# Kernel tuning notes

Measured on AMD Instinct MI355X. Metric: run time of the kernel, lower is better.

Reference implementation:

```python
import jax, jax.numpy as jnp
import numpy as np

B, C, S, DIM = 8, 3, 1024, 768
H = 3
HD = DIM // H  # 256


def setup_inputs() -> dict:
    key = jax.random.key(0)
    ks = jax.random.split(key, 7)
    s = 1.0 / np.sqrt(HD)  # torch Linear default init scale
    return {
        "linear_embed": jax.random.normal(ks[0], (B, C, S, DIM), dtype=jnp.float32),
        "Wq": jax.random.uniform(ks[1], (H, HD, HD), jnp.float32, -s, s),
        "bq": jax.random.uniform(ks[2], (H, HD), jnp.float32, -s, s),
        "Wk": jax.random.uniform(ks[3], (H, HD, HD), jnp.float32, -s, s),
        "bk": jax.random.uniform(ks[4], (H, HD), jnp.float32, -s, s),
        "Wv": jax.random.uniform(ks[5], (H, HD, HD), jnp.float32, -s, s),
        "bv": jax.random.uniform(ks[6], (H, HD), jnp.float32, -s, s),
    }


def reference(linear_embed, Wq, bq, Wk, bk, Wv, bv):
    # Split last dim into heads: [B, C, S, H, HD]
    x = linear_embed.reshape(B, C, S, H, HD)
    # Per-head Linear: y = x @ W.T + b (torch convention, W is [out, in])
    q = jnp.einsum("bcshd,hed->bcshe", x, Wq) + bq
    k = jnp.einsum("bcshd,hed->bcshe", x, Wk) + bk
    v = jnp.einsum("bcshd,hed->bcshe", x, Wv) + bv
    scale = 1.0 / np.sqrt(HD)
    scores = jnp.einsum("bcshe,bcthe->bchst", q, k) * scale  # [B,C,H,S,S]
    attn = jax.nn.softmax(scores, axis=-1)
    out = jnp.einsum("bchst,bcthe->bcshe", attn, v)  # [B,C,S,H,HD]
    # hstack over heads -> [B,C,S,DIM]; hstack over channels -> [B,S,C*DIM]
    out = out.reshape(B, C, S, DIM)
    return jnp.transpose(out, (0, 2, 1, 3)).reshape(B, S, C * DIM)
```

## Files before the change

### kernel.cpp

```cpp
#include <hip/hip_runtime.h>

#define Bn 8
#define Cn 3
#define Sn 1024
#define DIMn 768
#define Hn 3
#define HDn 256
#define BCHn 72
#define SnHD (Sn*HDn)

typedef __bf16 bf16x8 __attribute__((ext_vector_type(8)));
typedef float f32x4 __attribute__((ext_vector_type(4)));
typedef float f32x16 __attribute__((ext_vector_type(16)));
typedef unsigned short u16x8 __attribute__((ext_vector_type(8)));
typedef unsigned short u16x4 __attribute__((ext_vector_type(4)));
typedef unsigned u32x2 __attribute__((ext_vector_type(2)));
typedef unsigned u32x4 __attribute__((ext_vector_type(4)));

static __device__ __forceinline__ unsigned short f2bf(float f){
  unsigned u = __builtin_bit_cast(unsigned, f);
  u += 0x7fffu + ((u >> 16) & 1u);
  return (unsigned short)(u >> 16);
}
static __device__ __forceinline__ unsigned pk2(float a, float b){
  return (unsigned)f2bf(a) | ((unsigned)f2bf(b) << 16);
}
static __device__ __forceinline__ u16x4 cvt4(float4 v){
  u16x4 r = { f2bf(v.x), f2bf(v.y), f2bf(v.z), f2bf(v.w) };
  return r;
}
static __device__ __forceinline__ bf16x8 ld8(const void* p){
  return __builtin_bit_cast(bf16x8, *(const u16x8*)p);
}
static __device__ __forceinline__ float fexp2(float x){
#if __has_builtin(__builtin_amdgcn_exp2f)
  return __builtin_amdgcn_exp2f(x);
#else
  return exp2f(x);
#endif
}

#if __has_builtin(__builtin_amdgcn_global_load_lds)
#define HAVE_ASYNC 1
static __device__ __forceinline__ void async16(const void* g, void* l){
  __builtin_amdgcn_global_load_lds((const __attribute__((address_space(1))) void*)g,
                                   (__attribute__((address_space(3))) void*)l, 16, 0, 0);
}
#else
#define HAVE_ASYNC 0
#endif

static __device__ __forceinline__ bf16x8 pack8(const float* t, int hi){
  unsigned A0 = pk2(t[0], t[1]), A1 = pk2(t[2], t[3]);
  unsigned B0 = pk2(t[4], t[5]), B1 = pk2(t[6], t[7]);
#if __has_builtin(__builtin_amdgcn_permlane32_swap)
  u32x2 r0 = __builtin_amdgcn_permlane32_swap(A0, B0, false, false);
  u32x2 r1 = __builtin_amdgcn_permlane32_swap(A1, B1, false, false);
  u32x4 w = { r0[0], r1[0], r0[1], r1[1] };
#else
  unsigned sA0 = (unsigned)__shfl_xor((int)A0, 32), sA1 = (unsigned)__shfl_xor((int)A1, 32);
  unsigned sB0 = (unsigned)__shfl_xor((int)B0, 32), sB1 = (unsigned)__shfl_xor((int)B1, 32);
  u32x4 w = { hi ? sB0 : A0, hi ? sB1 : A1, hi ? B0 : sA0, hi ? B1 : sA1 };
#endif
  (void)hi;
  return __builtin_bit_cast(bf16x8, w);
}

__global__ __launch_bounds__(256) void wprep(
    const float* __restrict__ Wq, const float* __restrict__ Wk, const float* __restrict__ Wv,
    unsigned short* __restrict__ Wb)
{
  const int which = blockIdx.z, h = blockIdx.y;
  const float* src = which == 0 ? Wq : (which == 1 ? Wk : Wv);
  const float scale = (which == 0) ? 0.09016844136545405f : 1.0f;
  const int off = blockIdx.x*1024 + threadIdx.x*4;
  float4 v = *(const float4*)(src + (long)h*65536 + off);
  v.x *= scale; v.y *= scale; v.z *= scale; v.w *= scale;
  long o;
  if (which == 0){
    const int e = off >> 8, k0 = off & 255;
    const int ks = k0 >> 6, kst = (k0 >> 4) & 3, hb = (k0 >> 3) & 1, j0 = k0 & 7;
    o = (long)h*65536 + ks*16384 + ((e>>5)*4 + kst)*512 + (((hb<<5)|(e&31))*8) + j0;
  } else {
    o = (long)(which*Hn + h)*65536 + off;
  }
  *(u16x4*)(Wb + o) = cvt4(v);
}

__global__ __launch_bounds__(256, 2) void projkv(
    const float* __restrict__ x, const unsigned short* __restrict__ Wb,
    const float* __restrict__ bk, const float* __restrict__ bv,
    unsigned short* __restrict__ Kw, unsigned short* __restrict__ Vt)
{
  __shared__ alignas(16) unsigned short SM[23040];
  unsigned short* XA  = SM;
  unsigned short* WkL = SM + 2560;
  unsigned short* WvL = SM + 12800;
  unsigned short* TK  = SM;
  unsigned short* TV  = SM;

  const int tid = threadIdx.x, lane = tid & 63, wave = tid >> 6;
  const int l15 = lane & 15, quad = lane >> 4;
  const int bch = blockIdx.y;
  const int h = bch % Hn, c = (bch / Hn) % Cn, b = bch / (Hn*Cn);
  const int tb = blockIdx.x * 64;
  const long xb_ = ((long)(b*Cn + c)*Sn + tb)*DIMn + h*HDn;
  const unsigned short* Wkb = Wb + (long)(1*Hn + h)*65536;
  const unsigned short* Wvb = Wb + (long)(2*Hn + h)*65536;

  float4 xr[2]; u16x8 wk[4], wv[4];
  auto loadg = [&](int ks){
    const int k0 = ks*32;
    #pragma unroll
    for (int i = 0; i < 2; ++i){
      int id = tid + i*256;
      xr[i] = *(const float4*)(x + xb_ + (long)(id>>3)*DIMn + k0 + (id&7)*4);
    }
    #pragma unroll
    for (int i = 0; i < 4; ++i){
      int id = tid + i*256;
      wk[i] = *(const u16x8*)(Wkb + (id>>2)*HDn + k0 + (id&3)*8);
      wv[i] = *(const u16x8*)(Wvb + (id>>2)*HDn + k0 + (id&3)*8);
    }
  };
  loadg(0);

  f32x4 Ka[16] = {}; f32x4 Va[4][4] = {};
  for (int ks = 0; ks < 8; ++ks){
    #pragma unroll
    for (int i = 0; i < 2; ++i){
      int id = tid + i*256;
      *(u16x4*)&XA[(id>>3)*40 + (id&7)*4] = cvt4(xr[i]);
    }
    #pragma unroll
    for (int i = 0; i < 4; ++i){
      int id = tid + i*256;
      *(u16x8*)&WkL[(id>>2)*40 + (id&3)*8] = wk[i];
      *(u16x8*)&WvL[(id>>2)*40 + (id&3)*8] = wv[i];
    }
    __syncthreads();
    if (ks < 7) loadg(ks + 1);
    bf16x8 af = ld8(&XA[(wave*16 + l15)*40 + quad*8]);
    #pragma unroll
    for (int nt = 0; nt < 16; ++nt){
      bf16x8 bw = ld8(&WkL[(nt*16 + l15)*40 + quad*8]);
      Ka[nt] = __builtin_amdgcn_mfma_f32_16x16x32_bf16(af, bw, Ka[nt], 0, 0, 0);
    }
    bf16x8 avf[4], bxf[4];
    #pragma unroll
    for (int j = 0; j < 4; ++j) avf[j] = ld8(&WvL[((wave*4 + j)*16 + l15)*40 + quad*8]);
    #pragma unroll
    for (int n = 0; n < 4; ++n) bxf[n] = ld8(&XA[(n*16 + l15)*40 + quad*8]);
    #pragma unroll
    for (int j = 0; j < 4; ++j)
      #pragma unroll
      for (int n = 0; n < 4; ++n)
        Va[j][n] = __builtin_amdgcn_mfma_f32_16x16x32_bf16(avf[j], bxf[n], Va[j][n], 0, 0, 0);
    __syncthreads();
  }

  const float* bkh = bk + h*HDn;
  const float* bvh = bv + h*HDn;
  #pragma unroll
  for (int nt = 0; nt < 16; ++nt){
    const float bb = bkh[nt*16 + l15];
    #pragma unroll
    for (int r = 0; r < 4; ++r)
      TK[(wave*16 + quad*4 + r)*264 + nt*16 + l15] = f2bf(Ka[nt][r] + bb);
  }
  __syncthreads();
  {
    unsigned short* Kg = Kw + (long)bch*SnHD + (long)(tb>>5)*8192;
    #pragma unroll
    for (int i = 0; i < 8; ++i){
      const int f = wave*8 + i;
      const int tl = f >> 4, kc = f & 15;
      *(u16x8*)(Kg + (long)tl*8192 + kc*512 + lane*8) =
        *(const u16x8*)&TK[(tl*32 + (lane&31))*264 + kc*16 + (lane>>5)*8];
    }
  }
  __syncthreads();
  #pragma unroll
  for (int j = 0; j < 4; ++j){
    #pragma unroll
    for (int n = 0; n < 4; ++n){
      #pragma unroll
      for (int r = 0; r < 4; ++r){
        const int er = wave*64 + j*16 + quad*4 + r;
        TV[er*72 + n*16 + l15] = f2bf(Va[j][n][r] + bvh[er]);
      }
    }
  }
  __syncthreads();
  {
    unsigned short* Vg = Vt + (long)bch*SnHD + (long)(tb>>5)*8192;
    #pragma unroll
    for (int i = 0; i < 8; ++i){
      const int f = wave*8 + i;
      const int tcl = f >> 4, r2 = f & 15;
      *(u16x8*)(Vg + (long)tcl*8192 + r2*512 + lane*8) =
        *(const u16x8*)&TV[((r2>>1)*32 + (lane&31))*72 + tcl*32 + (r2&1)*16 + (lane>>5)*8];
    }
  }
}

__global__ __launch_bounds__(256, 2) void attn(
    const float* __restrict__ x, const unsigned short* __restrict__ Wb,
    const float* __restrict__ bq,
    const unsigned short* __restrict__ Kw, const unsigned short* __restrict__ Vt,
    float* __restrict__ out)
{
  __shared__ alignas(16) char SM[66560];

  const int tid = threadIdx.x, lane = tid & 63, wave = tid >> 6;
  const int l31 = lane & 31, hi = lane >> 5;
  const int bid = blockIdx.x;
  const int g = bid >> 3;
  const int bch = (g & ~7) | (bid & 7);
  const int qt = g & 7;
  const int h = bch % Hn, c = (bch / Hn) % Cn, b = bch / (Hn*Cn);
  const int q0 = qt * 128;
  const long xb_ = ((long)(b*Cn + c)*Sn + q0)*DIMn + h*HDn;

  float* bql = (float*)(SM + 65536);
  bql[tid] = bq[h*HDn + tid] * 0.09016844136545405f;

  float4 xv[4][2];
  auto loadX = [&](int ks){
    #pragma unroll
    for (int i = 0; i < 4; ++i){
      const int vid = tid + i*256;
      const int q = vid >> 3, kg = vid & 7;
      const float* p = x + xb_ + (long)q*DIMn + ks*64 + kg*8;
      xv[i][0] = *(const float4*)p;
      xv[i][1] = *(const float4*)(p + 4);
    }
  };
  const unsigned short* Wq2 = Wb + (long)h*65536;
  auto issueW = [&](int ks){
    #pragma unroll
    for (int i = 0; i < 8; ++i){
      const int f = wave*8 + i;
#if HAVE_ASYNC
      async16(Wq2 + (long)ks*16384 + f*512 + lane*8, SM + 16384 + f*1024);
#else
      *(u16x8*)(SM + 16384 + f*1024 + lane*16) =
          *(const u16x8*)(Wq2 + (long)ks*16384 + f*512 + lane*8);
#endif
    }
  };
  loadX(0);
  f32x16 acc[8] = {};
  for (int ks = 0; ks < 4; ++ks){
    #pragma unroll
    for (int i = 0; i < 4; ++i){
      const int vid = tid + i*256;
      const int q = vid >> 3, kg = vid & 7;
      u16x4 lo = cvt4(xv[i][0]), hh = cvt4(xv[i][1]);
      u16x8 w = { lo[0], lo[1], lo[2], lo[3], hh[0], hh[1], hh[2], hh[3] };
      *(u16x8*)(SM + q*128 + ((kg*16) ^ ((q & 7) << 4))) = w;
    }
    issueW(ks);
    __syncthreads();
    if (ks < 3) loadX(ks + 1);
    #pragma unroll
    for (int kst = 0; kst < 4; ++kst){
      bf16x8 xb = ld8(SM + (wave*32 + l31)*128 + ((kst*32 + hi*16) ^ ((l31 & 7) << 4)));
      #pragma unroll
      for (int et = 0; et < 8; ++et){
        bf16x8 af = ld8(SM + 16384 + (et*4 + kst)*1024 + lane*16);
        acc[et] = __builtin_amdgcn_mfma_f32_32x32x16_bf16(af, xb, acc[et], 0, 0, 0);
      }
    }
    __syncthreads();
  }

  const unsigned short* Kb = Kw + (long)bch*SnHD;
  const unsigned short* Vb = Vt + (long)bch*SnHD;
  auto stageKV = [&](int jt, int buf){
    const long kb2 = (long)jt * 8192;
    #pragma unroll
    for (int i = 0; i < 4; ++i){
      const int f = wave*4 + i;
#if HAVE_ASYNC
      async16(Kb + kb2 + f*512 + lane*8, SM + buf*16384 + f*1024);
#else
      *(u16x8*)(SM + buf*16384 + f*1024 + lane*16) = *(const u16x8*)(Kb + kb2 + f*512 + lane*8);
#endif
    }
    #pragma unroll
    for (int i = 0; i < 4; ++i){
      const int f = wave*4 + i;
#if HAVE_ASYNC
      async16(Vb + kb2 + f*512 + lane*8, SM + 32768 + buf*16384 + f*1024);
#else
      *(u16x8*)(SM + 32768 + buf*16384 + f*1024 + lane*16) = *(const u16x8*)(Vb + kb2 + f*512 + lane*8);
#endif
    }
  };
  stageKV(0, 0);

  bf16x8 qf[16];
  #pragma unroll
  for (int et = 0; et < 8; ++et){
    float t[16];
    #pragma unroll
    for (int G = 0; G < 4; ++G){
      f32x4 bb = *(const f32x4*)&bql[et*32 + 8*G + 4*hi];
      t[4*G+0] = acc[et][4*G+0] + bb[0];
      t[4*G+1] = acc[et][4*G+1] + bb[1];
      t[4*G+2] = acc[et][4*G+2] + bb[2];
      t[4*G+3] = acc[et][4*G+3] + bb[3];
    }
    qf[2*et]   = pack8(t,     hi);
    qf[2*et+1] = pack8(t + 8, hi);
  }
  __syncthreads();

  f32x16 o[8] = {};
  float lsum = 0.f;
  #pragma unroll 2
  for (int jt = 0; jt < 32; ++jt){
    const int buf = jt & 1;
    if (jt < 31) stageKV(jt + 1, buf ^ 1);
    f32x16 s = {};
    const char* KLb = SM + buf*16384 + lane*16;
    #pragma unroll
    for (int kc = 0; kc < 16; ++kc){
      bf16x8 kf = ld8(KLb + kc*1024);
      s = __builtin_amdgcn_mfma_f32_32x32x16_bf16(kf, qf[kc], s, 0, 0, 0);
    }
    float p[16];
    #pragma unroll
    for (int i = 0; i < 16; ++i) p[i] = fexp2(s[i]);
    lsum += (((p[0]+p[1])+(p[2]+p[3])) + ((p[4]+p[5])+(p[6]+p[7])))
          + (((p[8]+p[9])+(p[10]+p[11])) + ((p[12]+p[13])+(p[14]+p[15])));
    bf16x8 pB0 = pack8(p, hi), pB1 = pack8(p + 8, hi);
    const char* VLb = SM + 32768 + buf*16384 + lane*16;
    #pragma unroll
    for (int et = 0; et < 8; ++et){
      bf16x8 v0 = ld8(VLb + (et*2+0)*1024);
      o[et] = __builtin_amdgcn_mfma_f32_32x32x16_bf16(v0, pB0, o[et], 0, 0, 0);
      bf16x8 v1 = ld8(VLb + (et*2+1)*1024);
      o[et] = __builtin_amdgcn_mfma_f32_32x32x16_bf16(v1, pB1, o[et], 0, 0, 0);
    }
    __syncthreads();
  }

  const float lt = lsum + __shfl_xor(lsum, 32);
  const float inv = 1.0f / lt;
  #pragma unroll
  for (int et = 0; et < 8; ++et)
    #pragma unroll
    for (int r = 0; r < 16; ++r) o[et][r] *= inv;

  char* TB = SM + wave*16384;
  #pragma unroll
  for (int pass = 0; pass < 2; ++pass){
    #pragma unroll
    for (int e2 = 0; e2 < 4; ++e2){
      const int et = pass*4 + e2;
      #pragma unroll
      for (int G = 0; G < 4; ++G){
        f32x4 w = { o[et][4*G+0], o[et][4*G+1], o[et][4*G+2], o[et][4*G+3] };
        const int el0 = e2*32 + 8*G + 4*hi;
        *(f32x4*)(TB + l31*512 + ((el0*4) ^ ((l31 & 7) << 4))) = w;
      }
    }
    #pragma unroll
    for (int i = 0; i < 16; ++i){
      const int qr = i*2 + hi;
      f32x4 v = *(const f32x4*)(TB + qr*512 + ((l31*16) ^ ((qr & 7) << 4)));
      float* op = out + ((long)(b*Sn + q0 + wave*32 + qr)*Cn + c)*DIMn + h*HDn + pass*128 + l31*4;
      *(f32x4*)op = v;
    }
  }
}

extern "C" void kernel_launch(void* const* d_in, const int* in_sizes, int n_in,
                              void* d_out, int out_size, void* d_ws, size_t ws_size,
                              hipStream_t stream) {
  const float* x  = (const float*)d_in[0];
  const float* Wq = (const float*)d_in[1];
  const float* bq = (const float*)d_in[2];
  const float* Wk = (const float*)d_in[3];
  const float* bk = (const float*)d_in[4];
  const float* Wv = (const float*)d_in[5];
  const float* bv = (const float*)d_in[6];
  float* out = (float*)d_out;
  unsigned short* Kw = (unsigned short*)d_ws;
  unsigned short* Vt = Kw + (size_t)BCHn * SnHD;
  unsigned short* Wb = Vt + (size_t)BCHn * SnHD;

  wprep<<<dim3(64, Hn, 3), 256, 0, stream>>>(Wq, Wk, Wv, Wb);
  projkv<<<dim3(16, BCHn), 256, 0, stream>>>(x, Wb, bk, bv, Kw, Vt);
  attn<<<dim3(BCHn * 8), 256, 0, stream>>>(x, Wb, bq, Kw, Vt, out);
}
```

Baseline: 304.3 us.

## Restructure K/V projection with 32x32 MFMA and direct fragment-layout stores

The K/V projection kernel now uses 32x32x16 MFMAs with weights pre-swizzled by wprep into fragment layout and read straight from global memory. Outputs are packed and written directly in the attention kernel's layout, which removes the LDS transpose staging and several barriers. The attention kernel splits the QK^T accumulation into two independent chains to shorten MFMA dependency stalls, and interleaves exp with the PV MFMAs. It also drops the LDS bias buffer in favour of a fused fma on global loads. Reading weights from global per k-step could add memory traffic, and the two-chain split needs two accumulators instead of one.

```diff
diff --git a/kernel.cpp b/kernel.cpp
--- a/kernel.cpp
+++ b/kernel.cpp
@@ -27,6 +27,11 @@
 }
 static __device__ __forceinline__ u16x4 cvt4(float4 v){
   u16x4 r = { f2bf(v.x), f2bf(v.y), f2bf(v.z), f2bf(v.w) };
+  return r;
+}
+static __device__ __forceinline__ u16x8 cvt8(float4 a, float4 b){
+  u16x8 r = { f2bf(a.x), f2bf(a.y), f2bf(a.z), f2bf(a.w),
+              f2bf(b.x), f2bf(b.y), f2bf(b.z), f2bf(b.w) };
   return r;
 }
 static __device__ __forceinline__ bf16x8 ld8(const void* p){
@@ -76,14 +81,10 @@
   const int off = blockIdx.x*1024 + threadIdx.x*4;
   float4 v = *(const float4*)(src + (long)h*65536 + off);
   v.x *= scale; v.y *= scale; v.z *= scale; v.w *= scale;
-  long o;
-  if (which == 0){
-    const int e = off >> 8, k0 = off & 255;
-    const int ks = k0 >> 6, kst = (k0 >> 4) & 3, hb = (k0 >> 3) & 1, j0 = k0 & 7;
-    o = (long)h*65536 + ks*16384 + ((e>>5)*4 + kst)*512 + (((hb<<5)|(e&31))*8) + j0;
-  } else {
-    o = (long)(which*Hn + h)*65536 + off;
-  }
+  const int e = off >> 8, k0 = off & 255;
+  const int ks = k0 >> 6, kst = (k0 >> 4) & 3, hb = (k0 >> 3) & 1, j0 = k0 & 7;
+  const long o = (long)(which*Hn + h)*65536 + ks*16384
+               + ((e>>5)*4 + kst)*512 + (((hb<<5)|(e&31))*8) + j0;
   *(u16x4*)(Wb + o) = cvt4(v);
 }
 
@@ -92,15 +93,11 @@
     const float* __restrict__ bk, const float* __restrict__ bv,
     unsigned short* __restrict__ Kw, unsigned short* __restrict__ Vt)
 {
-  __shared__ alignas(16) unsigned short SM[23040];
-  unsigned short* XA  = SM;
-  unsigned short* WkL = SM + 2560;
-  unsigned short* WvL = SM + 12800;
-  unsigned short* TK  = SM;
-  unsigned short* TV  = SM;
+  __shared__ alignas(16) char SM[16384];
 
   const int tid = threadIdx.x, lane = tid & 63, wave = tid >> 6;
-  const int l15 = lane & 15, quad = lane >> 4;
+  const int l31 = lane & 31, hi = lane >> 5;
+  const int tg = wave >> 1, eh = wave & 1;
   const int bch = blockIdx.y;
   const int h = bch % Hn, c = (bch / Hn) % Cn, b = bch / (Hn*Cn);
   const int tb = blockIdx.x * 64;
@@ -108,98 +105,77 @@
   const unsigned short* Wkb = Wb + (long)(1*Hn + h)*65536;
   const unsigned short* Wvb = Wb + (long)(2*Hn + h)*65536;
 
-  float4 xr[2]; u16x8 wk[4], wv[4];
-  auto loadg = [&](int ks){
-    const int k0 = ks*32;
+  float4 xr[2][2];
+  auto loadX = [&](int ks){
     #pragma unroll
     for (int i = 0; i < 2; ++i){
-      int id = tid + i*256;
-      xr[i] = *(const float4*)(x + xb_ + (long)(id>>3)*DIMn + k0 + (id&7)*4);
-    }
-    #pragma unroll
-    for (int i = 0; i < 4; ++i){
-      int id = tid + i*256;
-      wk[i] = *(const u16x8*)(Wkb + (id>>2)*HDn + k0 + (id&3)*8);
-      wv[i] = *(const u16x8*)(Wvb + (id>>2)*HDn + k0 + (id&3)*8);
+      const int vid = tid + i*256;
+      const int t = vid >> 3, kg = vid & 7;
+      const float* p = x + xb_ + (long)t*DIMn + ks*64 + kg*8;
+      xr[i][0] = *(const float4*)p;
+      xr[i][1] = *(const float4*)(p + 4);
     }
   };
-  loadg(0);
-
-  f32x4 Ka[16] = {}; f32x4 Va[4][4] = {};
-  for (int ks = 0; ks < 8; ++ks){
+  loadX(0);
+
+  f32x16 accK[4] = {}, accV[4] = {};
+  for (int ks = 0; ks < 4; ++ks){
+    const int buf = ks & 1;
     #pragma unroll
     for (int i = 0; i < 2; ++i){
-      int id = tid + i*256;
-      *(u16x4*)&XA[(id>>3)*40 + (id&7)*4] = cvt4(xr[i]);
-    }
-    #pragma unroll
-    for (int i = 0; i < 4; ++i){
-      int id = tid + i*256;
-      *(u16x8*)&WkL[(id>>2)*40 + (id&3)*8] = wk[i];
-      *(u16x8*)&WvL[(id>>2)*40 + (id&3)*8] = wv[i];
+      const int vid = tid + i*256;
+      const int t = vid >> 3, kg = vid & 7;
+      *(u16x8*)(SM + buf*8192 + t*128 + ((kg*16) ^ ((t & 7) << 4))) = cvt8(xr[i][0], xr[i][1]);
     }
     __syncthreads();
-    if (ks < 7) loadg(ks + 1);
-    bf16x8 af = ld8(&XA[(wave*16 + l15)*40 + quad*8]);
-    #pragma unroll
-    for (int nt = 0; nt < 16; ++nt){
-      bf16x8 bw = ld8(&WkL[(nt*16 + l15)*40 + quad*8]);
-      Ka[nt] = __builtin_amdgcn_mfma_f32_16x16x32_bf16(af, bw, Ka[nt], 0, 0, 0);
-    }
-    bf16x8 avf[4], bxf[4];
-    #pragma unroll
-    for (int j = 0; j < 4; ++j) avf[j] = ld8(&WvL[((wave*4 + j)*16 + l15)*40 + quad*8]);
-    #pragma unroll
-    for (int n = 0; n < 4; ++n) bxf[n] = ld8(&XA[(n*16 + l15)*40 + quad*8]);
-    #pragma unroll
-    for (int j = 0; j < 4; ++j)
-      #pragma unroll
-      for (int n = 0; n < 4; ++n)
-        Va[j][n] = __builtin_amdgcn_mfma_f32_16x16x32_bf16(avf[j], bxf[n], Va[j][n], 0, 0, 0);
-    __syncthreads();
-  }
-
-  const float* bkh = bk + h*HDn;
-  const float* bvh = bv + h*HDn;
-  #pragma unroll
-  for (int nt = 0; nt < 16; ++nt){
-    const float bb = bkh[nt*16 + l15];
-    #pragma unroll
-    for (int r = 0; r < 4; ++r)
-      TK[(wave*16 + quad*4 + r)*264 + nt*16 + l15] = f2bf(Ka[nt][r] + bb);
-  }
-  __syncthreads();
+    if (ks < 3) loadX(ks + 1);
+    #pragma unroll
+    for (int kst = 0; kst < 4; ++kst){
+      bf16x8 wk2[4], wv2[4];
+      #pragma unroll
+      for (int et = 0; et < 4; ++et){
+        const long wo = (long)ks*16384 + ((eh*4 + et)*4 + kst)*512 + lane*8;
+        wk2[et] = ld8(Wkb + wo);
+        wv2[et] = ld8(Wvb + wo);
+      }
+      bf16x8 xf = ld8(SM + buf*8192 + (tg*32 + l31)*128 + ((kst*32 + hi*16) ^ ((l31 & 7) << 4)));
+      #pragma unroll
+      for (int et = 0; et < 4; ++et){
+        accK[et] = __builtin_amdgcn_mfma_f32_32x32x16_bf16(wk2[et], xf, accK[et], 0, 0, 0);
+        accV[et] = __builtin_amdgcn_mfma_f32_32x32x16_bf16(xf, wv2[et], accV[et], 0, 0, 0);
+      }
+    }
+  }
+
+  const int ttile = blockIdx.x*2 + tg;
   {
-    unsigned short* Kg = Kw + (long)bch*SnHD + (long)(tb>>5)*8192;
-    #pragma unroll
-    for (int i = 0; i < 8; ++i){
-      const int f = wave*8 + i;
-      const int tl = f >> 4, kc = f & 15;
-      *(u16x8*)(Kg + (long)tl*8192 + kc*512 + lane*8) =
-        *(const u16x8*)&TK[(tl*32 + (lane&31))*264 + kc*16 + (lane>>5)*8];
-    }
-  }
-  __syncthreads();
-  #pragma unroll
-  for (int j = 0; j < 4; ++j){
-    #pragma unroll
-    for (int n = 0; n < 4; ++n){
-      #pragma unroll
-      for (int r = 0; r < 4; ++r){
-        const int er = wave*64 + j*16 + quad*4 + r;
-        TV[er*72 + n*16 + l15] = f2bf(Va[j][n][r] + bvh[er]);
-      }
-    }
-  }
-  __syncthreads();
+    unsigned short* Kg = Kw + (long)bch*SnHD + (long)ttile*8192;
+    const float* bkh = bk + h*HDn + eh*128;
+    #pragma unroll
+    for (int et = 0; et < 4; ++et){
+      float tt[16];
+      #pragma unroll
+      for (int G = 0; G < 4; ++G){
+        const float4 bb = *(const float4*)(bkh + et*32 + 8*G + 4*hi);
+        tt[4*G+0] = accK[et][4*G+0] + bb.x;
+        tt[4*G+1] = accK[et][4*G+1] + bb.y;
+        tt[4*G+2] = accK[et][4*G+2] + bb.z;
+        tt[4*G+3] = accK[et][4*G+3] + bb.w;
+      }
+      *(u16x8*)(Kg + (eh*8 + et*2 + 0)*512 + lane*8) = __builtin_bit_cast(u16x8, pack8(tt,     hi));
+      *(u16x8*)(Kg + (eh*8 + et*2 + 1)*512 + lane*8) = __builtin_bit_cast(u16x8, pack8(tt + 8, hi));
+    }
+  }
   {
-    unsigned short* Vg = Vt + (long)bch*SnHD + (long)(tb>>5)*8192;
-    #pragma unroll
-    for (int i = 0; i < 8; ++i){
-      const int f = wave*8 + i;
-      const int tcl = f >> 4, r2 = f & 15;
-      *(u16x8*)(Vg + (long)tcl*8192 + r2*512 + lane*8) =
-        *(const u16x8*)&TV[((r2>>1)*32 + (lane&31))*72 + tcl*32 + (r2&1)*16 + (lane>>5)*8];
+    unsigned short* Vg = Vt + (long)bch*SnHD + (long)ttile*8192;
+    #pragma unroll
+    for (int et = 0; et < 4; ++et){
+      const float bs = bv[h*HDn + eh*128 + et*32 + l31];
+      float tt[16];
+      #pragma unroll
+      for (int r = 0; r < 16; ++r) tt[r] = accV[et][r] + bs;
+      *(u16x8*)(Vg + ((eh*4 + et)*2 + 0)*512 + lane*8) = __builtin_bit_cast(u16x8, pack8(tt,     hi));
+      *(u16x8*)(Vg + ((eh*4 + et)*2 + 1)*512 + lane*8) = __builtin_bit_cast(u16x8, pack8(tt + 8, hi));
     }
   }
 }
@@ -210,7 +186,7 @@
     const unsigned short* __restrict__ Kw, const unsigned short* __restrict__ Vt,
     float* __restrict__ out)
 {
-  __shared__ alignas(16) char SM[66560];
+  __shared__ alignas(16) char SM[65536];
 
   const int tid = threadIdx.x, lane = tid & 63, wave = tid >> 6;
   const int l31 = lane & 31, hi = lane >> 5;
@@ -222,9 +198,6 @@
   const int q0 = qt * 128;
   const long xb_ = ((long)(b*Cn + c)*Sn + q0)*DIMn + h*HDn;
 
-  float* bql = (float*)(SM + 65536);
-  bql[tid] = bq[h*HDn + tid] * 0.09016844136545405f;
-
   float4 xv[4][2];
   auto loadX = [&](int ks){
     #pragma unroll
@@ -256,9 +229,7 @@
     for (int i = 0; i < 4; ++i){
       const int vid = tid + i*256;
       const int q = vid >> 3, kg = vid & 7;
-      u16x4 lo = cvt4(xv[i][0]), hh = cvt4(xv[i][1]);
-      u16x8 w = { lo[0], lo[1], lo[2], lo[3], hh[0], hh[1], hh[2], hh[3] };
-      *(u16x8*)(SM + q*128 + ((kg*16) ^ ((q & 7) << 4))) = w;
+      *(u16x8*)(SM + q*128 + ((kg*16) ^ ((q & 7) << 4))) = cvt8(xv[i][0], xv[i][1]);
     }
     issueW(ks);
     __syncthreads();
@@ -300,17 +271,19 @@
   };
   stageKV(0, 0);
 
+  const float s2 = 0.09016844136545405f;
+  const float* bqh = bq + h*HDn;
   bf16x8 qf[16];
   #pragma unroll
   for (int et = 0; et < 8; ++et){
     float t[16];
     #pragma unroll
     for (int G = 0; G < 4; ++G){
-      f32x4 bb = *(const f32x4*)&bql[et*32 + 8*G + 4*hi];
-      t[4*G+0] = acc[et][4*G+0] + bb[0];
-      t[4*G+1] = acc[et][4*G+1] + bb[1];
-      t[4*G+2] = acc[et][4*G+2] + bb[2];
-      t[4*G+3] = acc[et][4*G+3] + bb[3];
+      const float4 bb = *(const float4*)(bqh + et*32 + 8*G + 4*hi);
+      t[4*G+0] = fmaf(bb.x, s2, acc[et][4*G+0]);
+      t[4*G+1] = fmaf(bb.y, s2, acc[et][4*G+1]);
+      t[4*G+2] = fmaf(bb.z, s2, acc[et][4*G+2]);
+      t[4*G+3] = fmaf(bb.w, s2, acc[et][4*G+3]);
     }
     qf[2*et]   = pack8(t,     hi);
     qf[2*et+1] = pack8(t + 8, hi);
@@ -323,27 +296,35 @@
   for (int jt = 0; jt < 32; ++jt){
     const int buf = jt & 1;
     if (jt < 31) stageKV(jt + 1, buf ^ 1);
-    f32x16 s = {};
+    f32x16 s0 = {}, s1 = {};
     const char* KLb = SM + buf*16384 + lane*16;
     #pragma unroll
-    for (int kc = 0; kc < 16; ++kc){
-      bf16x8 kf = ld8(KLb + kc*1024);
-      s = __builtin_amdgcn_mfma_f32_32x32x16_bf16(kf, qf[kc], s, 0, 0, 0);
-    }
+    for (int kc = 0; kc < 8; ++kc){
+      bf16x8 k0 = ld8(KLb + (2*kc+0)*1024);
+      s0 = __builtin_amdgcn_mfma_f32_32x32x16_bf16(k0, qf[2*kc+0], s0, 0, 0, 0);
+      bf16x8 k1 = ld8(KLb + (2*kc+1)*1024);
+      s1 = __builtin_amdgcn_mfma_f32_32x32x16_bf16(k1, qf[2*kc+1], s1, 0, 0, 0);
+    }
+    const char* VLb = SM + 32768 + buf*16384 + lane*16;
     float p[16];
     #pragma unroll
-    for (int i = 0; i < 16; ++i) p[i] = fexp2(s[i]);
-    lsum += (((p[0]+p[1])+(p[2]+p[3])) + ((p[4]+p[5])+(p[6]+p[7])))
-          + (((p[8]+p[9])+(p[10]+p[11])) + ((p[12]+p[13])+(p[14]+p[15])));
-    bf16x8 pB0 = pack8(p, hi), pB1 = pack8(p + 8, hi);
-    const char* VLb = SM + 32768 + buf*16384 + lane*16;
+    for (int i = 0; i < 8; ++i) p[i] = fexp2(s0[i] + s1[i]);
+    bf16x8 pB0 = pack8(p, hi);
     #pragma unroll
     for (int et = 0; et < 8; ++et){
       bf16x8 v0 = ld8(VLb + (et*2+0)*1024);
       o[et] = __builtin_amdgcn_mfma_f32_32x32x16_bf16(v0, pB0, o[et], 0, 0, 0);
+    }
+    #pragma unroll
+    for (int i = 8; i < 16; ++i) p[i] = fexp2(s0[i] + s1[i]);
+    bf16x8 pB1 = pack8(p + 8, hi);
+    #pragma unroll
+    for (int et = 0; et < 8; ++et){
       bf16x8 v1 = ld8(VLb + (et*2+1)*1024);
       o[et] = __builtin_amdgcn_mfma_f32_32x32x16_bf16(v1, pB1, o[et], 0, 0, 0);
     }
+    lsum += (((p[0]+p[1])+(p[2]+p[3])) + ((p[4]+p[5])+(p[6]+p[7])))
+          + (((p[8]+p[9])+(p[10]+p[11])) + ((p[12]+p[13])+(p[14]+p[15])));
     __syncthreads();
   }
 
```

Result: slower. 344.1 us (+13.1%).
